# Optimization experiments

Hardware: AMD Instinct MI355X
Metric: run time of the kernel (lower is better)

Reference implementation:

```python
import jax, jax.numpy as jnp
import numpy as np

V, D, DI, S, B, NI = 32000, 1024, 768, 512, 8, 197
EPS = 1e-5

def _ln(x, g, b):
    m = jnp.mean(x, axis=-1, keepdims=True)
    v = jnp.var(x, axis=-1, keepdims=True)
    return (x - m) * jax.lax.rsqrt(v + EPS) * g + b

def _pos_enc(seq_len, d):
    pos = np.arange(seq_len)[:, None].astype(np.float32)
    i = np.arange(0, d, 2).astype(np.float32)
    ang = pos / np.power(10000.0, i / d)
    pe = np.zeros((seq_len, d), dtype=np.float32)
    pe[:, 0::2] = np.sin(ang)
    pe[:, 1::2] = np.cos(ang)
    return jnp.asarray(pe)

def setup_inputs() -> dict:
    key = jax.random.key(0)
    ks = jax.random.split(key, 24)
    def rn(k, shape, scale=0.02):
        return jax.random.normal(k, shape, dtype=jnp.float32) * scale
    return {
        'tokens': jax.random.randint(ks[0], (B, S), 0, V),
        'img_emb': jax.random.normal(ks[1], (B, NI, DI), dtype=jnp.float32),
        'emb_table': rn(ks[2], (V, D), 1.0),
        'Wq1': rn(ks[3], (D, D)), 'bq1': jnp.zeros((D,), jnp.float32),
        'Wk1': rn(ks[4], (D, D)), 'bk1': jnp.zeros((D,), jnp.float32),
        'Wv1': rn(ks[5], (D, D)), 'bv1': jnp.zeros((D,), jnp.float32),
        'g1': jnp.ones((D,), jnp.float32), 'b1': jnp.zeros((D,), jnp.float32),
        'Wq2': rn(ks[6], (D, D)), 'bq2': jnp.zeros((D,), jnp.float32),
        'Wk2': rn(ks[7], (DI, D)), 'bk2': jnp.zeros((D,), jnp.float32),
        'Wv2': rn(ks[8], (DI, D)), 'bv2': jnp.zeros((D,), jnp.float32),
        'g2': jnp.ones((D,), jnp.float32), 'b2': jnp.zeros((D,), jnp.float32),
        'Wp': rn(ks[9], (D, V)), 'bp': jnp.zeros((V,), jnp.float32),
    }

def _forward(tokens, img_emb, emb_table, Wq1, bq1, Wk1, bk1, Wv1, bv1, g1, b1,
             Wq2, bq2, Wk2, bk2, Wv2, bv2, g2, b2, Wp, bp):
    scale = 1.0 / jnp.sqrt(jnp.float32(D))
    x = emb_table[tokens] + _pos_enc(S, D)[None]  # [B,S,D]
    # masked (causal) self-attention
    Q = x @ Wq1 + bq1
    K = x @ Wk1 + bk1
    Vv = x @ Wv1 + bv1
    attn = jnp.einsum('bqd,bkd->bqk', Q, K) * scale
    causal = jnp.tril(jnp.ones((S, S), dtype=bool))
    attn = jnp.where(causal[None], attn, -jnp.inf)
    A = jax.nn.softmax(attn, axis=-1)
    x = _ln(A @ Vv + x, g1, b1)
    # cross-attention over image tokens
    Q2 = x @ Wq2 + bq2
    K2 = img_emb @ Wk2 + bk2
    V2 = img_emb @ Wv2 + bv2
    A2 = jax.nn.softmax(jnp.einsum('bqd,bkd->bqk', Q2, K2) * scale, axis=-1)
    x = _ln(A2 @ V2 + x, g2, b2)
    # vocab projection (note: Decoder.forward never calls self.ff)
    return x @ Wp + bp  # [B,S,V]

def reference(tokens, img_emb, emb_table, Wq1, bq1, Wk1, bk1, Wv1, bv1, g1, b1,
              Wq2, bq2, Wk2, bk2, Wv2, bv2, g2, b2, Wp, bp):
    return _forward(tokens, img_emb, emb_table, Wq1, bq1, Wk1, bk1, Wv1, bv1, g1, b1,
                    Wq2, bq2, Wk2, bk2, Wv2, bv2, g2, b2, Wp, bp)
```

## Files before the change

### kernel.cpp

```cpp
#include <hip/hip_runtime.h>
#include <hip/hip_bf16.h>


#define DEV __device__ __forceinline__

typedef __bf16 bf16x8 __attribute__((ext_vector_type(8)));
typedef float f32x4 __attribute__((ext_vector_type(4)));
typedef unsigned int u32;
typedef __hip_bfloat16 bf16;

DEV void llds16(const void* g, void* l) {
  __builtin_amdgcn_global_load_lds((const __attribute__((address_space(1))) u32*)g,
                                   (__attribute__((address_space(3))) u32*)l, 16, 0, 0);
}

DEV float wredsum(float v){
#pragma unroll
  for (int o = 32; o; o >>= 1) v += __shfl_xor(v, o, 64);
  return v;
}
DEV float wredmax(float v){
#pragma unroll
  for (int o = 32; o; o >>= 1) v = fmaxf(v, __shfl_xor(v, o, 64));
  return v;
}

DEV void store_out(float* p, float v){ *p = v; }
DEV void store_out(bf16* p, float v){ *p = __float2bfloat16(v); }

__global__ __launch_bounds__(512, 1) void gemm256_kernel(
    const bf16* __restrict__ A, const bf16* __restrict__ Bt, float* __restrict__ C,
    const float* __restrict__ bias, int M, int N, int K, int lda, int ldb, int ldc)
{
  __shared__ alignas(16) char lds[131072];
  const int tid  = threadIdx.x;
  const int wave = tid >> 6, lane = tid & 63;
  const int lo = lane & 15, hi = lane >> 4;
  const int hi2 = hi ^ ((lo >> 1) & 3);
  const int wr = wave >> 2, wc = wave & 3;
  const int koff = (((lane & 3) ^ ((lane >> 3) & 3)) << 3);

  const int nbx = M >> 8, nby = N >> 8;
  const int nwg = nbx * nby;
  int id = blockIdx.x;
  int g = (nwg & 7) ? id : ((id & 7) * (nwg >> 3) + (id >> 3));
  const int row0 = (g % nbx) * 256;
  const int col0 = (g / nbx) * 256;
  const int srow = lane >> 2;
  const int NT = K >> 5;

  auto stageA = [&](int t) {
    char* base = lds + (t & 3) * 32768;
    const int kk = (t << 5) + koff;
#pragma unroll
    for (int j = 0; j < 2; j++) {
      const int r = (j * 8 + wave) * 16 + srow;
      llds16(A + (long)(row0 + r) * lda + kk, base + (j * 8 + wave) * 1024);
    }
  };
  auto stageB = [&](int t) {
    char* base = lds + (t & 3) * 32768 + 16384;
    const int kk = (t << 5) + koff;
#pragma unroll
    for (int j = 0; j < 2; j++) {
      const int r = (j * 8 + wave) * 16 + srow;
      llds16(Bt + (long)(col0 + r) * ldb + kk, base + (j * 8 + wave) * 1024);
    }
  };

  stageA(0); stageB(0);
  stageA(1); stageB(1);
  stageA(2); stageB(2);
  asm volatile("s_waitcnt vmcnt(8)" ::: "memory");
  __builtin_amdgcn_s_barrier();
  asm volatile("" ::: "memory");

  f32x4 acc[8][4] = {};

  for (int t = 0; t < NT; t++) {
    char* As = lds + (t & 3) * 32768;
    char* Bs = As + 16384;
    bf16x8 af[4], bfv[4];
#pragma unroll
    for (int m = 0; m < 4; m++)
      af[m] = *(const bf16x8*)(As + ((wr * 128 + m * 16 + lo) << 6) + (hi2 << 4));
#pragma unroll
    for (int n = 0; n < 4; n++)
      bfv[n] = *(const bf16x8*)(Bs + ((wc * 64 + n * 16 + lo) << 6) + (hi2 << 4));
    if (t + 3 < NT) stageA(t + 3);
    __builtin_amdgcn_s_setprio(1);
#pragma unroll
    for (int m = 0; m < 4; m++)
#pragma unroll
      for (int n = 0; n < 4; n++)
        acc[m][n] = __builtin_amdgcn_mfma_f32_16x16x32_bf16(af[m], bfv[n], acc[m][n], 0, 0, 0);
    __builtin_amdgcn_s_setprio(0);
    asm volatile("" ::: "memory");
    __builtin_amdgcn_s_barrier();
    asm volatile("" ::: "memory");
#pragma unroll
    for (int m = 0; m < 4; m++)
      af[m] = *(const bf16x8*)(As + ((wr * 128 + (m + 4) * 16 + lo) << 6) + (hi2 << 4));
    if (t + 3 < NT) stageB(t + 3);
    __builtin_amdgcn_s_setprio(1);
#pragma unroll
    for (int m = 0; m < 4; m++)
#pragma unroll
      for (int n = 0; n < 4; n++)
        acc[m + 4][n] = __builtin_amdgcn_mfma_f32_16x16x32_bf16(af[m], bfv[n], acc[m + 4][n], 0, 0, 0);
    __builtin_amdgcn_s_setprio(0);
    if (t < NT - 3)       asm volatile("s_waitcnt vmcnt(8)" ::: "memory");
    else if (t == NT - 3) asm volatile("s_waitcnt vmcnt(4)" ::: "memory");
    else                  asm volatile("s_waitcnt vmcnt(0)" ::: "memory");
    __builtin_amdgcn_s_barrier();
    asm volatile("" ::: "memory");
  }

#pragma unroll
  for (int m = 0; m < 8; m++) {
    const int r = row0 + wr * 128 + m * 16 + hi * 4;
#pragma unroll
    for (int n = 0; n < 4; n++) {
      const int c = col0 + wc * 64 + n * 16 + lo;
      const float bb = bias ? bias[c] : 0.0f;
#pragma unroll
      for (int j = 0; j < 4; j++)
        C[(long)(r + j) * ldc + c] = acc[m][n][j] + bb;
    }
  }
}

template<typename OutT>
__global__ __launch_bounds__(256) void gemm_bt_kernel(
    const bf16* __restrict__ A, const bf16* __restrict__ Bt, OutT* __restrict__ C,
    const float* __restrict__ bias, int M, int N, int K,
    int lda, int ldb, int ldc, long sA, long sB, long sC)
{
  A  += (long)blockIdx.z * sA;
  Bt += (long)blockIdx.z * sB;
  C  += (long)blockIdx.z * sC;
  __shared__ alignas(16) bf16 As[128*32];
  __shared__ alignas(16) bf16 Bs[128*32];
  const int tid = threadIdx.x;
  const int wave = tid >> 6, lane = tid & 63;
  const int lo = lane & 15, hi = lane >> 4;
  const int hi2 = hi ^ ((lo >> 1) & 3);
  const int wr = wave >> 1, wc = wave & 1;
  const int row0 = blockIdx.x * 128, col0 = blockIdx.y * 128;
  const int srow  = lane >> 2;
  const int skoff = (((lane & 3) ^ ((lane >> 3) & 3)) << 3);

  f32x4 acc[4][4] = {};

  for (int k0 = 0; k0 < K; k0 += 32) {
#pragma unroll
    for (int c = 0; c < 2; ++c) {
      const int seg = c*4 + wave;
      int ra = row0 + seg*16 + srow; ra = ra < M ? ra : M-1;
      llds16(A + (long)ra*lda + (k0 + skoff), (char*)As + seg*1024);
      int rb = col0 + seg*16 + srow; rb = rb < N ? rb : N-1;
      llds16(Bt + (long)rb*ldb + (k0 + skoff), (char*)Bs + seg*1024);
    }
    __syncthreads();
    bf16x8 af[4], bfv[4];
#pragma unroll
    for (int m = 0; m < 4; m++)
      af[m] = *(const bf16x8*)((const char*)As + (wr*64 + m*16 + lo)*64 + hi2*16);
#pragma unroll
    for (int n = 0; n < 4; n++)
      bfv[n] = *(const bf16x8*)((const char*)Bs + (wc*64 + n*16 + lo)*64 + hi2*16);
#pragma unroll
    for (int m = 0; m < 4; m++)
#pragma unroll
      for (int n = 0; n < 4; n++)
        acc[m][n] = __builtin_amdgcn_mfma_f32_16x16x32_bf16(af[m], bfv[n], acc[m][n], 0, 0, 0);
    __syncthreads();
  }

#pragma unroll
  for (int m = 0; m < 4; m++) {
    const int rbase = row0 + wr*64 + m*16 + hi*4;
#pragma unroll
    for (int n = 0; n < 4; n++) {
      const int cc = col0 + wc*64 + n*16 + lo;
      if (cc >= N) continue;
      const float bb = bias ? bias[cc] : 0.0f;
#pragma unroll
      for (int j = 0; j < 4; j++) {
        const int rr = rbase + j;
        if (rr < M) store_out(&C[(long)rr*ldc + cc], acc[m][n][j] + bb);
      }
    }
  }
}

__global__ __launch_bounds__(256) void wprep_kernel(
    const float* __restrict__ W, bf16* __restrict__ Wt, int K, int N)
{
  __shared__ bf16 t[32][33];
  const int k0 = blockIdx.x * 32, n0 = blockIdx.y * 32;
  const int tx = threadIdx.x & 31, ty = threadIdx.x >> 5;
#pragma unroll
  for (int i = 0; i < 4; i++)
    t[ty + i*8][tx] = __float2bfloat16(W[(long)(k0 + ty + i*8)*N + n0 + tx]);
  __syncthreads();
#pragma unroll
  for (int i = 0; i < 4; i++)
    Wt[(long)(n0 + ty + i*8)*K + k0 + tx] = t[tx][ty + i*8];
}

__global__ __launch_bounds__(256) void transpose_pad_kernel(
    const bf16* __restrict__ in, bf16* __restrict__ out,
    int R, int Cc, int outLD, long inBatch, long outBatch)
{
  in  += (long)blockIdx.z * inBatch;
  out += (long)blockIdx.z * outBatch;
  __shared__ bf16 t[32][33];
  const int r0 = blockIdx.x * 32, c0 = blockIdx.y * 32;
  const int tx = threadIdx.x & 31, ty = threadIdx.x >> 5;
#pragma unroll
  for (int i = 0; i < 4; i++) {
    const int r = r0 + ty + i*8;
    bf16 v = __float2bfloat16(0.0f);
    if (r < R) v = in[(long)r*Cc + c0 + tx];
    t[ty + i*8][tx] = v;
  }
  __syncthreads();
#pragma unroll
  for (int i = 0; i < 4; i++) {
    const int oc = r0 + tx;
    const int orow = c0 + ty + i*8;
    if (oc < outLD) out[(long)orow*outLD + oc] = t[tx][ty + i*8];
  }
}

__global__ __launch_bounds__(256) void embed_kernel(
    const int* __restrict__ tok, const float* __restrict__ tbl,
    float* __restrict__ xf, bf16* __restrict__ xb)
{
  const int row = blockIdx.x;
  const int s = row & 511;
  const float pos = (float)s;
  const float* te = tbl + (long)tok[row] * 1024;
  const int d0 = threadIdx.x * 4;
  float4 v = *(const float4*)(te + d0);
  float o[4] = {v.x, v.y, v.z, v.w};
#pragma unroll
  for (int k = 0; k < 4; k++) {
    const int d = d0 + k;
    const int i2 = d & ~1;
    const float ang = pos * powf(10000.0f, -(float)i2 * (1.0f/1024.0f));
    o[k] += (d & 1) ? cosf(ang) : sinf(ang);
  }
  *(float4*)(xf + (long)row*1024 + d0) = make_float4(o[0], o[1], o[2], o[3]);
#pragma unroll
  for (int k = 0; k < 4; k++) xb[(long)row*1024 + d0 + k] = __float2bfloat16(o[k]);
}

__global__ __launch_bounds__(256) void cvt_bf16_kernel(const float* __restrict__ in, bf16* __restrict__ out, long n)
{
  long i = (long)blockIdx.x * blockDim.x + threadIdx.x;
  if (i < n) out[i] = __float2bfloat16(in[i]);
}

__global__ __launch_bounds__(64) void softmax_causal_kernel(
    const float* __restrict__ Sc, bf16* __restrict__ P)
{
  const int row = blockIdx.x;
  const int q = row & 511;
  const float* srow = Sc + (long)row * 512;
  bf16* prow = P + (long)row * 512;
  const int lane = threadIdx.x;
  const float scale = 0.03125f;
  float mx = -1e30f;
  for (int j = lane; j <= q; j += 64) mx = fmaxf(mx, srow[j]);
  mx = wredmax(mx);
  float sum = 0.0f;
  for (int j = lane; j <= q; j += 64) sum += expf((srow[j] - mx) * scale);
  sum = wredsum(sum);
  const float inv = 1.0f / sum;
  for (int j = lane; j < 512; j += 64) {
    float p = (j <= q) ? expf((srow[j] - mx) * scale) * inv : 0.0f;
    prow[j] = __float2bfloat16(p);
  }
}

__global__ __launch_bounds__(64) void softmax_cross_kernel(
    const float* __restrict__ Sc, bf16* __restrict__ P)
{
  const int row = blockIdx.x;
  const float* srow = Sc + (long)row * 224;
  bf16* prow = P + (long)row * 224;
  const int lane = threadIdx.x;
  const float scale = 0.03125f;
  float mx = -1e30f;
  for (int j = lane; j < 197; j += 64) mx = fmaxf(mx, srow[j]);
  mx = wredmax(mx);
  float sum = 0.0f;
  for (int j = lane; j < 197; j += 64) sum += expf((srow[j] - mx) * scale);
  sum = wredsum(sum);
  const float inv = 1.0f / sum;
  for (int j = lane; j < 224; j += 64) {
    float p = (j < 197) ? expf((srow[j] - mx) * scale) * inv : 0.0f;
    prow[j] = __float2bfloat16(p);
  }
}

__global__ __launch_bounds__(256) void add_ln_kernel(
    const float* __restrict__ Acc, const float* __restrict__ Res,
    const float* __restrict__ g, const float* __restrict__ b,
    float* __restrict__ outf, bf16* __restrict__ outb)
{
  const int row = blockIdx.x;
  const float* a = Acc + (long)row * 1024;
  const float* r = Res + (long)row * 1024;
  float vals[4], s = 0.0f, ss = 0.0f;
#pragma unroll
  for (int i = 0; i < 4; i++) {
    const int d = threadIdx.x + i*256;
    const float v = a[d] + r[d];
    vals[i] = v; s += v; ss += v*v;
  }
  s = wredsum(s); ss = wredsum(ss);
  __shared__ float sh[8];
  const int wave = threadIdx.x >> 6, lane = threadIdx.x & 63;
  if (lane == 0) { sh[wave] = s; sh[wave+4] = ss; }
  __syncthreads();
  s  = sh[0] + sh[1] + sh[2] + sh[3];
  ss = sh[4] + sh[5] + sh[6] + sh[7];
  const float mean = s * (1.0f/1024.0f);
  const float var  = ss * (1.0f/1024.0f) - mean*mean;
  const float inv  = rsqrtf(var + 1e-5f);
#pragma unroll
  for (int i = 0; i < 4; i++) {
    const int d = threadIdx.x + i*256;
    const float y = (vals[i] - mean) * inv * g[d] + b[d];
    if (outf) outf[(long)row*1024 + d] = y;
    outb[(long)row*1024 + d] = __float2bfloat16(y);
  }
}

extern "C" void kernel_launch(void* const* d_in, const int* in_sizes, int n_in,
                              void* d_out, int out_size, void* d_ws, size_t ws_size,
                              hipStream_t stream) {
  const int*   tokens = (const int*)  d_in[0];
  const float* img    = (const float*)d_in[1];
  const float* emb    = (const float*)d_in[2];
  const float* Wq1    = (const float*)d_in[3];
  const float* bq1    = (const float*)d_in[4];
  const float* Wk1    = (const float*)d_in[5];
  const float* bk1    = (const float*)d_in[6];
  const float* Wv1    = (const float*)d_in[7];
  const float* bv1    = (const float*)d_in[8];
  const float* g1     = (const float*)d_in[9];
  const float* b1     = (const float*)d_in[10];
  const float* Wq2    = (const float*)d_in[11];
  const float* bq2    = (const float*)d_in[12];
  const float* Wk2    = (const float*)d_in[13];
  const float* bk2    = (const float*)d_in[14];
  const float* Wv2    = (const float*)d_in[15];
  const float* bv2    = (const float*)d_in[16];
  const float* g2     = (const float*)d_in[17];
  const float* b2     = (const float*)d_in[18];
  const float* Wp     = (const float*)d_in[19];
  const float* bp     = (const float*)d_in[20];
  float* out = (float*)d_out;

  const int B = 8, S = 512, D = 1024, DI = 768, NI = 197, NIP = 224, V = 32000;
  const int M = B * S;
  const int MI = B * NI;

  char* ws = (char*)d_ws;
  size_t off = 0;
  auto alloc = [&](size_t bytes) -> char* {
    char* p = ws + off; off += (bytes + 255) & ~(size_t)255; return p;
  };
  bf16* Wq1t = (bf16*)alloc((size_t)D*D*2);
  bf16* Wk1t = (bf16*)alloc((size_t)D*D*2);
  bf16* Wv1t = (bf16*)alloc((size_t)D*D*2);
  bf16* Wq2t = (bf16*)alloc((size_t)D*D*2);
  bf16* Wk2t = (bf16*)alloc((size_t)D*DI*2);
  bf16* Wv2t = (bf16*)alloc((size_t)D*DI*2);
  bf16* Wpt  = (bf16*)alloc((size_t)V*D*2);
  float* xf  = (float*)alloc((size_t)M*D*4);
  bf16*  xb  = (bf16*) alloc((size_t)M*D*2);
  bf16*  imgb= (bf16*) alloc((size_t)MI*DI*2);
  bf16*  Q   = (bf16*) alloc((size_t)M*D*2);
  bf16*  Kb  = (bf16*) alloc((size_t)M*D*2);
  bf16*  Vb  = (bf16*) alloc((size_t)M*D*2);
  bf16*  Vt  = (bf16*) alloc((size_t)M*D*2);
  float* sc1 = (float*)alloc((size_t)B*S*S*4);
  bf16*  P1  = (bf16*) alloc((size_t)B*S*S*2);
  float* ao1 = (float*)alloc((size_t)M*D*4);
  float* x2f = (float*)alloc((size_t)M*D*4);
  bf16*  x2b = (bf16*) alloc((size_t)M*D*2);
  bf16*  Q2  = (bf16*) alloc((size_t)M*D*2);
  bf16*  K2  = (bf16*) alloc((size_t)MI*D*2);
  bf16*  V2  = (bf16*) alloc((size_t)MI*D*2);
  bf16*  V2t = (bf16*) alloc((size_t)B*D*NIP*2);
  float* sc2 = (float*)alloc((size_t)B*S*NIP*4);
  bf16*  P2  = (bf16*) alloc((size_t)B*S*NIP*2);
  float* ao2 = (float*)alloc((size_t)M*D*4);
  bf16*  x3b = (bf16*) alloc((size_t)M*D*2);
  (void)ws_size; (void)in_sizes; (void)n_in; (void)out_size;

  wprep_kernel<<<dim3(D/32,  D/32), 256, 0, stream>>>(Wq1, Wq1t, D, D);
  wprep_kernel<<<dim3(D/32,  D/32), 256, 0, stream>>>(Wk1, Wk1t, D, D);
  wprep_kernel<<<dim3(D/32,  D/32), 256, 0, stream>>>(Wv1, Wv1t, D, D);
  wprep_kernel<<<dim3(D/32,  D/32), 256, 0, stream>>>(Wq2, Wq2t, D, D);
  wprep_kernel<<<dim3(DI/32, D/32), 256, 0, stream>>>(Wk2, Wk2t, DI, D);
  wprep_kernel<<<dim3(DI/32, D/32), 256, 0, stream>>>(Wv2, Wv2t, DI, D);
  wprep_kernel<<<dim3(D/32,  V/32), 256, 0, stream>>>(Wp,  Wpt,  D, V);

  embed_kernel<<<M, 256, 0, stream>>>(tokens, emb, xf, xb);
  {
    long n = (long)MI * DI;
    cvt_bf16_kernel<<<(int)((n + 255)/256), 256, 0, stream>>>(img, imgb, n);
  }

  auto gemmF = [&](const bf16* A, const bf16* Bt, float* C, const float* bias,
                   int m, int n, int k, int lda, int ldb, int ldc,
                   long sA, long sB, long sC, int batch) {
    dim3 g((m+127)/128, (n+127)/128, batch);
    gemm_bt_kernel<float><<<g, 256, 0, stream>>>(A, Bt, C, bias, m, n, k, lda, ldb, ldc, sA, sB, sC);
  };
  auto gemmB = [&](const bf16* A, const bf16* Bt, bf16* C, const float* bias,
                   int m, int n, int k, int lda, int ldb, int ldc,
                   long sA, long sB, long sC, int batch) {
    dim3 g((m+127)/128, (n+127)/128, batch);
    gemm_bt_kernel<bf16><<<g, 256, 0, stream>>>(A, Bt, C, bias, m, n, k, lda, ldb, ldc, sA, sB, sC);
  };

  gemmB(xb, Wq1t, Q,  bq1, M, D, D, D, D, D, 0, 0, 0, 1);
  gemmB(xb, Wk1t, Kb, bk1, M, D, D, D, D, D, 0, 0, 0, 1);
  gemmB(xb, Wv1t, Vb, bv1, M, D, D, D, D, D, 0, 0, 0, 1);
  transpose_pad_kernel<<<dim3(S/32, D/32, B), 256, 0, stream>>>(
      Vb, Vt, S, D, S, (long)S*D, (long)D*S);
  gemmF(Q, Kb, sc1, nullptr, S, S, D, D, D, S, (long)S*D, (long)S*D, (long)S*S, B);
  softmax_causal_kernel<<<M, 64, 0, stream>>>(sc1, P1);
  gemmF(P1, Vt, ao1, nullptr, S, D, S, S, S, D, (long)S*S, (long)D*S, (long)S*D, B);
  add_ln_kernel<<<M, 256, 0, stream>>>(ao1, xf, g1, b1, x2f, x2b);

  gemmB(x2b, Wq2t, Q2, bq2, M, D, D, D, D, D, 0, 0, 0, 1);
  gemmB(imgb, Wk2t, K2, bk2, MI, D, DI, DI, DI, D, 0, 0, 0, 1);
  gemmB(imgb, Wv2t, V2, bv2, MI, D, DI, DI, DI, D, 0, 0, 0, 1);
  transpose_pad_kernel<<<dim3((NIP+31)/32, D/32, B), 256, 0, stream>>>(
      V2, V2t, NI, D, NIP, (long)NI*D, (long)D*NIP);
  gemmF(Q2, K2, sc2, nullptr, S, NI, D, D, D, NIP, (long)S*D, (long)NI*D, (long)S*NIP, B);
  softmax_cross_kernel<<<M, 64, 0, stream>>>(sc2, P2);
  gemmF(P2, V2t, ao2, nullptr, S, D, NIP, NIP, NIP, D, (long)S*NIP, (long)D*NIP, (long)S*D, B);
  add_ln_kernel<<<M, 256, 0, stream>>>(ao2, x2f, g2, b2, nullptr, x3b);

  {
    dim3 g((M/256) * (V/256));
    gemm256_kernel<<<g, 512, 0, stream>>>(x3b, Wpt, out, bp, M, V, D, D, D, V);
  }
}
```

Before: 792.5 us.

## Use 32x32 MFMA in vocab GEMM and fuse QKV and KV2 projection GEMMs

The 256x256 vocab-projection GEMM switches from 16x16x32 to 32x32x16 bf16 MFMA tiles. It loads all A and B fragments once per k-step, so the mid-iteration barrier goes away, and it adds sched_barriers. Separately, the Q/K/V self-attention projections become one GEMM with N=3D, and the cross-attention K/V projections become one GEMM with N=2D, using concatenated biases and strided views. The weight-prep launches are also batched into fewer kernels. The fused GEMMs assume the transposed weight buffers are allocated contiguously, which is a layout risk, and the single-barrier loop changes how LDS reads overlap with the prefetch.

```diff
diff --git a/kernel.cpp b/kernel.cpp
--- a/kernel.cpp
+++ b/kernel.cpp
@@ -6,6 +6,7 @@
 
 typedef __bf16 bf16x8 __attribute__((ext_vector_type(8)));
 typedef float f32x4 __attribute__((ext_vector_type(4)));
+typedef float f32x16 __attribute__((ext_vector_type(16)));
 typedef unsigned int u32;
 typedef __hip_bfloat16 bf16;
 
@@ -35,27 +36,25 @@
   __shared__ alignas(16) char lds[131072];
   const int tid  = threadIdx.x;
   const int wave = tid >> 6, lane = tid & 63;
-  const int lo = lane & 15, hi = lane >> 4;
-  const int hi2 = hi ^ ((lo >> 1) & 3);
+  const int l31 = lane & 31, lh = lane >> 5;
   const int wr = wave >> 2, wc = wave & 3;
   const int koff = (((lane & 3) ^ ((lane >> 3) & 3)) << 3);
 
-  const int nbx = M >> 8, nby = N >> 8;
-  const int nwg = nbx * nby;
+  const int nbx = M >> 8;
+  const int nwg = nbx * (N >> 8);
   int id = blockIdx.x;
   int g = (nwg & 7) ? id : ((id & 7) * (nwg >> 3) + (id >> 3));
-  const int row0 = (g % nbx) * 256;
-  const int col0 = (g / nbx) * 256;
+  const int row0 = (g % nbx) * 256, col0 = (g / nbx) * 256;
+  const int NT = K >> 5;
   const int srow = lane >> 2;
-  const int NT = K >> 5;
 
   auto stageA = [&](int t) {
     char* base = lds + (t & 3) * 32768;
     const int kk = (t << 5) + koff;
 #pragma unroll
     for (int j = 0; j < 2; j++) {
-      const int r = (j * 8 + wave) * 16 + srow;
-      llds16(A + (long)(row0 + r) * lda + kk, base + (j * 8 + wave) * 1024);
+      const int seg = j * 8 + wave;
+      llds16(A + (long)(row0 + seg * 16 + srow) * lda + kk, base + seg * 1024);
     }
   };
   auto stageB = [&](int t) {
@@ -63,69 +62,69 @@
     const int kk = (t << 5) + koff;
 #pragma unroll
     for (int j = 0; j < 2; j++) {
-      const int r = (j * 8 + wave) * 16 + srow;
-      llds16(Bt + (long)(col0 + r) * ldb + kk, base + (j * 8 + wave) * 1024);
+      const int seg = j * 8 + wave;
+      llds16(Bt + (long)(col0 + seg * 16 + srow) * ldb + kk, base + seg * 1024);
     }
   };
 
-  stageA(0); stageB(0);
-  stageA(1); stageB(1);
-  stageA(2); stageB(2);
+  f32x16 acc[4][2] = {};
+
+  stageA(0); stageB(0); stageA(1); stageB(1); stageA(2); stageB(2);
   asm volatile("s_waitcnt vmcnt(8)" ::: "memory");
   __builtin_amdgcn_s_barrier();
-  asm volatile("" ::: "memory");
-
-  f32x4 acc[8][4] = {};
+  __builtin_amdgcn_sched_barrier(0);
 
   for (int t = 0; t < NT; t++) {
-    char* As = lds + (t & 3) * 32768;
-    char* Bs = As + 16384;
-    bf16x8 af[4], bfv[4];
+    const char* As = lds + (t & 3) * 32768;
+    const char* Bs = As + 16384;
+    bf16x8 af[4][2], bfv[2][2];
+#pragma unroll
+    for (int m = 0; m < 4; m++) {
+      const int r = wr * 128 + m * 32 + l31;
+      const int key = (r >> 1) & 3;
+#pragma unroll
+      for (int ks = 0; ks < 2; ks++)
+        af[m][ks] = *(const bf16x8*)(As + (r << 6) + (((lh + 2 * ks) ^ key) << 4));
+    }
+#pragma unroll
+    for (int n = 0; n < 2; n++) {
+      const int r = wc * 64 + n * 32 + l31;
+      const int key = (r >> 1) & 3;
+#pragma unroll
+      for (int ks = 0; ks < 2; ks++)
+        bfv[n][ks] = *(const bf16x8*)(Bs + (r << 6) + (((lh + 2 * ks) ^ key) << 4));
+    }
+    if (t + 3 < NT) { stageA(t + 3); stageB(t + 3); }
+    __builtin_amdgcn_sched_barrier(0);
+    __builtin_amdgcn_s_setprio(1);
 #pragma unroll
     for (int m = 0; m < 4; m++)
-      af[m] = *(const bf16x8*)(As + ((wr * 128 + m * 16 + lo) << 6) + (hi2 << 4));
-#pragma unroll
-    for (int n = 0; n < 4; n++)
-      bfv[n] = *(const bf16x8*)(Bs + ((wc * 64 + n * 16 + lo) << 6) + (hi2 << 4));
-    if (t + 3 < NT) stageA(t + 3);
-    __builtin_amdgcn_s_setprio(1);
-#pragma unroll
-    for (int m = 0; m < 4; m++)
-#pragma unroll
-      for (int n = 0; n < 4; n++)
-        acc[m][n] = __builtin_amdgcn_mfma_f32_16x16x32_bf16(af[m], bfv[n], acc[m][n], 0, 0, 0);
+#pragma unroll
+      for (int n = 0; n < 2; n++)
+#pragma unroll
+        for (int ks = 0; ks < 2; ks++)
+          acc[m][n] = __builtin_amdgcn_mfma_f32_32x32x16_bf16(af[m][ks], bfv[n][ks], acc[m][n], 0, 0, 0);
     __builtin_amdgcn_s_setprio(0);
-    asm volatile("" ::: "memory");
-    __builtin_amdgcn_s_barrier();
-    asm volatile("" ::: "memory");
-#pragma unroll
-    for (int m = 0; m < 4; m++)
-      af[m] = *(const bf16x8*)(As + ((wr * 128 + (m + 4) * 16 + lo) << 6) + (hi2 << 4));
-    if (t + 3 < NT) stageB(t + 3);
-    __builtin_amdgcn_s_setprio(1);
-#pragma unroll
-    for (int m = 0; m < 4; m++)
-#pragma unroll
-      for (int n = 0; n < 4; n++)
-        acc[m + 4][n] = __builtin_amdgcn_mfma_f32_16x16x32_bf16(af[m], bfv[n], acc[m + 4][n], 0, 0, 0);
-    __builtin_amdgcn_s_setprio(0);
+    __builtin_amdgcn_sched_barrier(0);
     if (t < NT - 3)       asm volatile("s_waitcnt vmcnt(8)" ::: "memory");
     else if (t == NT - 3) asm volatile("s_waitcnt vmcnt(4)" ::: "memory");
     else                  asm volatile("s_waitcnt vmcnt(0)" ::: "memory");
     __builtin_amdgcn_s_barrier();
-    asm volatile("" ::: "memory");
-  }
-
-#pragma unroll
-  for (int m = 0; m < 8; m++) {
-    const int r = row0 + wr * 128 + m * 16 + hi * 4;
-#pragma unroll
-    for (int n = 0; n < 4; n++) {
-      const int c = col0 + wc * 64 + n * 16 + lo;
-      const float bb = bias ? bias[c] : 0.0f;
-#pragma unroll
-      for (int j = 0; j < 4; j++)
-        C[(long)(r + j) * ldc + c] = acc[m][n][j] + bb;
+    __builtin_amdgcn_sched_barrier(0);
+  }
+
+#pragma unroll
+  for (int n = 0; n < 2; n++) {
+    const int c = col0 + wc * 64 + n * 32 + l31;
+    const float bb = bias ? bias[c] : 0.0f;
+#pragma unroll
+    for (int m = 0; m < 4; m++) {
+      const int rb = row0 + wr * 128 + m * 32 + 4 * lh;
+#pragma unroll
+      for (int r = 0; r < 16; r++) {
+        const int row = rb + (r & 3) + 8 * (r >> 2);
+        C[(long)row * ldc + c] = acc[m][n][r] + bb;
+      }
     }
   }
 }
@@ -194,9 +193,13 @@
   }
 }
 
-__global__ __launch_bounds__(256) void wprep_kernel(
-    const float* __restrict__ W, bf16* __restrict__ Wt, int K, int N)
-{
+__global__ __launch_bounds__(256) void wprep4_kernel(
+    const float* W0, const float* W1, const float* W2, const float* W3,
+    bf16* T0, bf16* T1, bf16* T2, bf16* T3, int K, int N)
+{
+  const int z = blockIdx.z;
+  const float* W = z == 0 ? W0 : z == 1 ? W1 : z == 2 ? W2 : W3;
+  bf16* T = z == 0 ? T0 : z == 1 ? T1 : z == 2 ? T2 : T3;
   __shared__ bf16 t[32][33];
   const int k0 = blockIdx.x * 32, n0 = blockIdx.y * 32;
   const int tx = threadIdx.x & 31, ty = threadIdx.x >> 5;
@@ -206,12 +209,12 @@
   __syncthreads();
 #pragma unroll
   for (int i = 0; i < 4; i++)
-    Wt[(long)(n0 + ty + i*8)*K + k0 + tx] = t[tx][ty + i*8];
+    T[(long)(n0 + ty + i*8)*K + k0 + tx] = t[tx][ty + i*8];
 }
 
 __global__ __launch_bounds__(256) void transpose_pad_kernel(
     const bf16* __restrict__ in, bf16* __restrict__ out,
-    int R, int Cc, int outLD, long inBatch, long outBatch)
+    int R, int Cc, int inLD, int outLD, long inBatch, long outBatch)
 {
   in  += (long)blockIdx.z * inBatch;
   out += (long)blockIdx.z * outBatch;
@@ -222,7 +225,7 @@
   for (int i = 0; i < 4; i++) {
     const int r = r0 + ty + i*8;
     bf16 v = __float2bfloat16(0.0f);
-    if (r < R) v = in[(long)r*Cc + c0 + tx];
+    if (r < R) v = in[(long)r*inLD + c0 + tx];
     t[ty + i*8][tx] = v;
   }
   __syncthreads();
@@ -232,6 +235,14 @@
     const int orow = c0 + ty + i*8;
     if (oc < outLD) out[(long)orow*outLD + oc] = t[tx][ty + i*8];
   }
+}
+
+__global__ __launch_bounds__(256) void concat_bias_kernel(
+    const float* a, const float* b, const float* c, int n1, int n2, int n3, float* out)
+{
+  const int i = blockIdx.x * 256 + threadIdx.x;
+  if (i >= n1 + n2 + n3) return;
+  out[i] = i < n1 ? a[i] : (i < n1 + n2 ? b[i - n1] : c[i - n1 - n2]);
 }
 
 __global__ __launch_bounds__(256) void embed_kernel(
@@ -382,12 +393,12 @@
   bf16* Wk2t = (bf16*)alloc((size_t)D*DI*2);
   bf16* Wv2t = (bf16*)alloc((size_t)D*DI*2);
   bf16* Wpt  = (bf16*)alloc((size_t)V*D*2);
+  float* bqkv= (float*)alloc((size_t)3*D*4);
+  float* bkv2= (float*)alloc((size_t)2*D*4);
   float* xf  = (float*)alloc((size_t)M*D*4);
   bf16*  xb  = (bf16*) alloc((size_t)M*D*2);
   bf16*  imgb= (bf16*) alloc((size_t)MI*DI*2);
-  bf16*  Q   = (bf16*) alloc((size_t)M*D*2);
-  bf16*  Kb  = (bf16*) alloc((size_t)M*D*2);
-  bf16*  Vb  = (bf16*) alloc((size_t)M*D*2);
+  bf16*  QKV = (bf16*) alloc((size_t)M*3*D*2);
   bf16*  Vt  = (bf16*) alloc((size_t)M*D*2);
   float* sc1 = (float*)alloc((size_t)B*S*S*4);
   bf16*  P1  = (bf16*) alloc((size_t)B*S*S*2);
@@ -395,8 +406,7 @@
   float* x2f = (float*)alloc((size_t)M*D*4);
   bf16*  x2b = (bf16*) alloc((size_t)M*D*2);
   bf16*  Q2  = (bf16*) alloc((size_t)M*D*2);
-  bf16*  K2  = (bf16*) alloc((size_t)MI*D*2);
-  bf16*  V2  = (bf16*) alloc((size_t)MI*D*2);
+  bf16*  KV2 = (bf16*) alloc((size_t)MI*2*D*2);
   bf16*  V2t = (bf16*) alloc((size_t)B*D*NIP*2);
   float* sc2 = (float*)alloc((size_t)B*S*NIP*4);
   bf16*  P2  = (bf16*) alloc((size_t)B*S*NIP*2);
@@ -404,13 +414,11 @@
   bf16*  x3b = (bf16*) alloc((size_t)M*D*2);
   (void)ws_size; (void)in_sizes; (void)n_in; (void)out_size;
 
-  wprep_kernel<<<dim3(D/32,  D/32), 256, 0, stream>>>(Wq1, Wq1t, D, D);
-  wprep_kernel<<<dim3(D/32,  D/32), 256, 0, stream>>>(Wk1, Wk1t, D, D);
-  wprep_kernel<<<dim3(D/32,  D/32), 256, 0, stream>>>(Wv1, Wv1t, D, D);
-  wprep_kernel<<<dim3(D/32,  D/32), 256, 0, stream>>>(Wq2, Wq2t, D, D);
-  wprep_kernel<<<dim3(DI/32, D/32), 256, 0, stream>>>(Wk2, Wk2t, DI, D);
-  wprep_kernel<<<dim3(DI/32, D/32), 256, 0, stream>>>(Wv2, Wv2t, DI, D);
-  wprep_kernel<<<dim3(D/32,  V/32), 256, 0, stream>>>(Wp,  Wpt,  D, V);
+  wprep4_kernel<<<dim3(D/32,  D/32, 4), 256, 0, stream>>>(Wq1, Wk1, Wv1, Wq2, Wq1t, Wk1t, Wv1t, Wq2t, D, D);
+  wprep4_kernel<<<dim3(DI/32, D/32, 2), 256, 0, stream>>>(Wk2, Wv2, nullptr, nullptr, Wk2t, Wv2t, nullptr, nullptr, DI, D);
+  wprep4_kernel<<<dim3(D/32,  V/32, 1), 256, 0, stream>>>(Wp, nullptr, nullptr, nullptr, Wpt, nullptr, nullptr, nullptr, D, V);
+  concat_bias_kernel<<<(3*D+255)/256, 256, 0, stream>>>(bq1, bk1, bv1, D, D, D, bqkv);
+  concat_bias_kernel<<<(2*D+255)/256, 256, 0, stream>>>(bk2, bv2, nullptr, D, D, 0, bkv2);
 
   embed_kernel<<<M, 256, 0, stream>>>(tokens, emb, xf, xb);
   {
@@ -431,22 +439,19 @@
     gemm_bt_kernel<bf16><<<g, 256, 0, stream>>>(A, Bt, C, bias, m, n, k, lda, ldb, ldc, sA, sB, sC);
   };
 
-  gemmB(xb, Wq1t, Q,  bq1, M, D, D, D, D, D, 0, 0, 0, 1);
-  gemmB(xb, Wk1t, Kb, bk1, M, D, D, D, D, D, 0, 0, 0, 1);
-  gemmB(xb, Wv1t, Vb, bv1, M, D, D, D, D, D, 0, 0, 0, 1);
+  gemmB(xb, Wq1t, QKV, bqkv, M, 3*D, D, D, D, 3*D, 0, 0, 0, 1);
   transpose_pad_kernel<<<dim3(S/32, D/32, B), 256, 0, stream>>>(
-      Vb, Vt, S, D, S, (long)S*D, (long)D*S);
-  gemmF(Q, Kb, sc1, nullptr, S, S, D, D, D, S, (long)S*D, (long)S*D, (long)S*S, B);
+      QKV + 2*D, Vt, S, D, 3*D, S, (long)S*3*D, (long)D*S);
+  gemmF(QKV, QKV + D, sc1, nullptr, S, S, D, 3*D, 3*D, S, (long)S*3*D, (long)S*3*D, (long)S*S, B);
   softmax_causal_kernel<<<M, 64, 0, stream>>>(sc1, P1);
   gemmF(P1, Vt, ao1, nullptr, S, D, S, S, S, D, (long)S*S, (long)D*S, (long)S*D, B);
   add_ln_kernel<<<M, 256, 0, stream>>>(ao1, xf, g1, b1, x2f, x2b);
 
   gemmB(x2b, Wq2t, Q2, bq2, M, D, D, D, D, D, 0, 0, 0, 1);
-  gemmB(imgb, Wk2t, K2, bk2, MI, D, DI, DI, DI, D, 0, 0, 0, 1);
-  gemmB(imgb, Wv2t, V2, bv2, MI, D, DI, DI, DI, D, 0, 0, 0, 1);
+  gemmB(imgb, Wk2t, KV2, bkv2, MI, 2*D, DI, DI, DI, 2*D, 0, 0, 0, 1);
   transpose_pad_kernel<<<dim3((NIP+31)/32, D/32, B), 256, 0, stream>>>(
-      V2, V2t, NI, D, NIP, (long)NI*D, (long)D*NIP);
-  gemmF(Q2, K2, sc2, nullptr, S, NI, D, D, D, NIP, (long)S*D, (long)NI*D, (long)S*NIP, B);
+      KV2 + D, V2t, NI, D, 2*D, NIP, (long)NI*2*D, (long)D*NIP);
+  gemmF(Q2, KV2, sc2, nullptr, S, NI, D, D, 2*D, NIP, (long)S*D, (long)NI*2*D, (long)S*NIP, B);
   softmax_cross_kernel<<<M, 64, 0, stream>>>(sc2, P2);
   gemmF(P2, V2t, ao2, nullptr, S, D, NIP, NIP, NIP, D, (long)S*NIP, (long)D*NIP, (long)S*D, B);
   add_ln_kernel<<<M, 256, 0, stream>>>(ao2, x2f, g2, b2, nullptr, x3b);
```

New measurement: 722.7 us. 1.1x faster.
